# Performance work log

Measured on AMD Instinct MI355X. Metric: run time of the kernel, lower is better.

## Reference

```python
import jax, jax.numpy as jnp
import numpy as np

NUM_EXPERTS = 32
TOP_K = 4
HIDDEN = 2048
INTER = 768
N_TOKENS = 2048
NORM_TOPK = True


def setup_inputs() -> dict:
    key = jax.random.key(0)
    k0, k1, k2, k3 = jax.random.split(key, 4)
    hidden_states = jax.random.normal(k0, (N_TOKENS, HIDDEN), dtype=jnp.float32)
    # router gate: Linear(hidden, num_experts), stored as (h, E)
    Wg = jax.random.normal(k1, (HIDDEN, NUM_EXPERTS), dtype=jnp.float32) * 0.02
    # per-expert merged gate_up: (E, h, 2*i); down: (E, i, h)
    Wgu = jax.random.normal(k2, (NUM_EXPERTS, HIDDEN, 2 * INTER), dtype=jnp.float32) * 0.02
    Wd = jax.random.normal(k3, (NUM_EXPERTS, INTER, HIDDEN), dtype=jnp.float32) * 0.02
    return {"hidden_states": hidden_states, "Wg": Wg, "Wgu": Wgu, "Wd": Wd}


def reference(hidden_states, Wg, Wgu, Wd):
    E = Wgu.shape[0]
    # ---- routing ----
    router_logits = hidden_states @ Wg                       # (N, E)
    probs = jax.nn.softmax(router_logits.astype(jnp.float32), axis=-1)
    topk_w, topk_idx = jax.lax.top_k(probs, TOP_K)           # (N, K)
    if NORM_TOPK:
        topk_w = topk_w / jnp.sum(topk_w, axis=-1, keepdims=True)
    topk_w = topk_w.astype(hidden_states.dtype)
    # dense combine weights: (N, E), zero where expert not selected
    combine = jnp.einsum("nke,nk->ne", jax.nn.one_hot(topk_idx, E, dtype=topk_w.dtype), topk_w)
    # ---- experts (dense dispatch, zero-weighted combine == gather/scatter math) ----
    gate_up = jnp.einsum("nh,ehf->nef", hidden_states, Wgu)  # (N, E, 2i)
    gate, up = jnp.split(gate_up, 2, axis=-1)                # (N, E, i) each
    y = jax.nn.silu(gate) * up                               # SiluAndMul
    y = y * combine[:, :, None]                              # apply routing weight before down-proj (linear -> equivalent)
    out = jnp.einsum("nef,efh->nh", y, Wd)                   # (N, h)
    return out
```

## Files before the change

kernel.cpp:

```cpp
#include <hip/hip_runtime.h>
#include <hip/hip_bf16.h>

#define NE 32
#define TOPK 4
#define HID 2048
#define INTER 768
#define NT 2048
#define MAXTILE 96

typedef float f32x4 __attribute__((ext_vector_type(4)));
typedef float f32x2 __attribute__((ext_vector_type(2)));
typedef unsigned int u32x4 __attribute__((ext_vector_type(4)));
typedef unsigned int u32x2 __attribute__((ext_vector_type(2)));
typedef short short8 __attribute__((ext_vector_type(8)));
typedef __bf16 bf16x8 __attribute__((ext_vector_type(8)));

__device__ inline unsigned short f2bf(float f) {
  unsigned u = __builtin_bit_cast(unsigned, f);
  u += 0x7fffu + ((u >> 16) & 1u);
  return (unsigned short)(u >> 16);
}
__device__ inline unsigned pack2(unsigned short a, unsigned short b) {
  return (unsigned)a | ((unsigned)b << 16);
}
__device__ inline f32x4 mfma_bf16(short8 a, short8 b, f32x4 c) {
  return __builtin_amdgcn_mfma_f32_16x16x32_bf16(
      __builtin_bit_cast(bf16x8, a), __builtin_bit_cast(bf16x8, b), c, 0, 0, 0);
}
__device__ inline void gload16(const void* g, void* l) {
  __builtin_amdgcn_global_load_lds(
      (const __attribute__((address_space(1))) void*)g,
      (__attribute__((address_space(3))) void*)l, 16, 0, 0);
}
__device__ inline bool locate(const int* __restrict__ counts, int tile, int& e,
                              int& m0, int& base, int& ne) {
  int tl = tile;
  base = 0;
  for (e = 0; e < NE; ++e) {
    const int c = counts[e];
    const int nt = (c + 127) >> 7;
    if (tl < nt) {
      m0 = tl << 7;
      ne = c;
      return true;
    }
    tl -= nt;
    base += c;
  }
  return false;
}

__global__ __launch_bounds__(64) void k_router(const float* __restrict__ X,
                                               const float* __restrict__ Wg,
                                               int* __restrict__ expert_of,
                                               float* __restrict__ weight_of,
                                               int* __restrict__ counts,
                                               unsigned short* __restrict__ Xb) {
  const int n = blockIdx.x;
  const int lane = threadIdx.x;
  const float* x = X + (size_t)n * HID;
  float acc[NE];
#pragma unroll
  for (int e = 0; e < NE; ++e) acc[e] = 0.f;
  for (int h = lane; h < HID; h += 64) {
    const float xv = x[h];
    const f32x4* wr = (const f32x4*)(Wg + (size_t)h * NE);
#pragma unroll
    for (int q = 0; q < NE / 4; ++q) {
      f32x4 w4 = wr[q];
      acc[q * 4 + 0] += xv * w4[0];
      acc[q * 4 + 1] += xv * w4[1];
      acc[q * 4 + 2] += xv * w4[2];
      acc[q * 4 + 3] += xv * w4[3];
    }
  }
  const f32x4* x4 = (const f32x4*)x;
  u32x2* xb2 = (u32x2*)(Xb + (size_t)n * HID);
#pragma unroll
  for (int it = 0; it < HID / 4 / 64; ++it) {
    const int q = it * 64 + lane;
    f32x4 v = x4[q];
    u32x2 t = {pack2(f2bf(v[0]), f2bf(v[1])), pack2(f2bf(v[2]), f2bf(v[3]))};
    xb2[q] = t;
  }
#pragma unroll
  for (int off = 32; off >= 1; off >>= 1) {
#pragma unroll
    for (int e = 0; e < NE; ++e) acc[e] += __shfl_xor(acc[e], off, 64);
  }
  if (lane == 0) {
    float m = acc[0];
#pragma unroll
    for (int e = 1; e < NE; ++e) m = fmaxf(m, acc[e]);
    unsigned used = 0;
    int idx[TOPK];
    float wv[TOPK];
    float wsum = 0.f;
    for (int k = 0; k < TOPK; ++k) {
      int best = 0;
      float bv = -1e30f;
      for (int e = 0; e < NE; ++e) {
        if (!((used >> e) & 1u) && acc[e] > bv) { bv = acc[e]; best = e; }
      }
      used |= 1u << best;
      float w = expf(bv - m);
      idx[k] = best;
      wv[k] = w;
      wsum += w;
    }
    const float inv = 1.f / wsum;
    for (int k = 0; k < TOPK; ++k) {
      expert_of[n * TOPK + k] = idx[k];
      weight_of[n * TOPK + k] = wv[k] * inv;
      atomicAdd(&counts[idx[k]], 1);
    }
  }
}

__global__ __launch_bounds__(64) void k_scatter(const int* __restrict__ expert_of,
                                                const float* __restrict__ weight_of,
                                                const int* __restrict__ counts,
                                                int* __restrict__ slot_token,
                                                float* __restrict__ slot_w) {
  const int e = blockIdx.x;
  const int lane = threadIdx.x;
  int cnt = 0;
  for (int i = 0; i < NE; ++i) cnt += (i < e) ? counts[i] : 0;
  for (int a0 = 0; a0 < NT * TOPK; a0 += 64) {
    const int a = a0 + lane;
    const bool m = (expert_of[a] == e);
    const unsigned long long bal = __ballot(m);
    if (m) {
      const int pos = cnt + __popcll(bal & ((1ull << lane) - 1ull));
      slot_token[pos] = a >> 2;
      slot_w[pos] = weight_of[a];
    }
    cnt += __popcll(bal);
  }
}

__global__ __launch_bounds__(512, 4) void k_gemm1(
    const unsigned short* __restrict__ Xb, const float* __restrict__ Wgu,
    const int* __restrict__ slot_token, const float* __restrict__ slot_w,
    const int* __restrict__ counts, unsigned short* __restrict__ Y) {
  int e, m0, base, ne;
  if (!locate(counts, blockIdx.x, e, m0, base, ne)) return;
  const int n0 = blockIdx.y * 64;
  const int tid = threadIdx.x;
  const int lane = tid & 63, w = tid >> 6;
  const int wm = w >> 1, wn = w & 1;
  const int fr = lane & 15, fo = lane >> 4;
  const int lr = lane >> 3, lk = lane & 7;

  __shared__ __attribute__((aligned(16))) unsigned short As[2][128 * 64];
  __shared__ __attribute__((aligned(16))) unsigned short Bg[2][64 * 64];
  __shared__ __attribute__((aligned(16))) unsigned short Bu[2][64 * 64];

  f32x4 accg[2][2], accu[2][2];
#pragma unroll
  for (int i = 0; i < 2; ++i)
#pragma unroll
    for (int j = 0; j < 2; ++j) {
      f32x4 z = {0.f, 0.f, 0.f, 0.f};
      accg[i][j] = z;
      accu[i][j] = z;
    }

  const unsigned short* asrc[2];
#pragma unroll
  for (int i = 0; i < 2; ++i) {
    const int ra = (w * 2 + i) * 8 + lr;
    const int tok = slot_token[base + min(m0 + ra, ne - 1)];
    asrc[i] = Xb + (size_t)tok * HID + ((lk ^ (ra & 7)) << 3);
  }

  const int np = tid & 31, kg = (tid >> 5) & 7, rg = tid >> 8;
  const float* bsrc = Wgu + (size_t)e * HID * (2 * INTER) +
                      (size_t)(kg * 8) * (2 * INTER) + rg * INTER + n0 + 2 * np;
  const int n_a = 2 * np, n_b = 2 * np + 1;
  const int wofa = n_a * 64 + ((kg ^ (n_a & 7)) << 3);
  const int wofb = n_b * 64 + ((kg ^ (n_b & 7)) << 3);

  auto stage_a = [&](int t, int b) {
#pragma unroll
    for (int i = 0; i < 2; ++i) gload16(asrc[i] + t * 64, &As[b][(w * 2 + i) * 512]);
  };
  auto load_b = [&](int t, f32x2* bv) {
    const float* bp = bsrc + (size_t)(t * 64) * (2 * INTER);
#pragma unroll
    for (int j = 0; j < 8; ++j) bv[j] = *(const f32x2*)(bp + (size_t)j * (2 * INTER));
  };
  auto pack_write = [&](const f32x2* bv, int b) {
    u32x4 ta = {pack2(f2bf(bv[0][0]), f2bf(bv[1][0])), pack2(f2bf(bv[2][0]), f2bf(bv[3][0])),
                pack2(f2bf(bv[4][0]), f2bf(bv[5][0])), pack2(f2bf(bv[6][0]), f2bf(bv[7][0]))};
    u32x4 tb = {pack2(f2bf(bv[0][1]), f2bf(bv[1][1])), pack2(f2bf(bv[2][1]), f2bf(bv[3][1])),
                pack2(f2bf(bv[4][1]), f2bf(bv[5][1])), pack2(f2bf(bv[6][1]), f2bf(bv[7][1]))};
    unsigned short* Bd = rg ? Bu[b] : Bg[b];
    *(u32x4*)&Bd[wofa] = ta;
    *(u32x4*)&Bd[wofb] = tb;
  };
  auto do_mfma = [&](int b) {
#pragma unroll
    for (int ks = 0; ks < 2; ++ks) {
      const int c = ks * 4 + fo;
      short8 a[2], bg[2], bu[2];
#pragma unroll
      for (int mi = 0; mi < 2; ++mi) {
        const int row = wm * 32 + mi * 16 + fr;
        a[mi] = *(const short8*)&As[b][row * 64 + ((c ^ (row & 7)) << 3)];
      }
#pragma unroll
      for (int ni = 0; ni < 2; ++ni) {
        const int row = wn * 32 + ni * 16 + fr;
        const int off = row * 64 + ((c ^ (row & 7)) << 3);
        bg[ni] = *(const short8*)&Bg[b][off];
        bu[ni] = *(const short8*)&Bu[b][off];
      }
#pragma unroll
      for (int mi = 0; mi < 2; ++mi)
#pragma unroll
        for (int ni = 0; ni < 2; ++ni) {
          accg[mi][ni] = mfma_bf16(a[mi], bg[ni], accg[mi][ni]);
          accu[mi][ni] = mfma_bf16(a[mi], bu[ni], accu[mi][ni]);
        }
    }
  };

  const int NS = HID / 64;
  f32x2 bv[2][8];
  stage_a(0, 0);
  load_b(0, bv[0]);
  load_b(1, bv[1]);
  pack_write(bv[0], 0);
  asm volatile("s_waitcnt lgkmcnt(0)" ::: "memory");
  __builtin_amdgcn_s_barrier();

#pragma unroll 2
  for (int t = 0; t < NS - 2; ++t) {
    const int cur = t & 1, nxt = cur ^ 1;
    stage_a(t + 1, nxt);
    load_b(t + 2, bv[cur]);
    asm volatile("s_waitcnt vmcnt(18)" ::: "memory");
    do_mfma(cur);
    pack_write(bv[nxt], nxt);
    asm volatile("s_waitcnt lgkmcnt(0)" ::: "memory");
    __builtin_amdgcn_s_barrier();
  }
  {
    const int t = NS - 2, cur = t & 1, nxt = cur ^ 1;
    stage_a(t + 1, nxt);
    asm volatile("s_waitcnt vmcnt(10)" ::: "memory");
    do_mfma(cur);
    pack_write(bv[nxt], nxt);
    __syncthreads();
  }
  do_mfma((NS - 1) & 1);

#pragma unroll
  for (int mi = 0; mi < 2; ++mi) {
#pragma unroll
    for (int j = 0; j < 4; ++j) {
      const int gm = m0 + wm * 32 + mi * 16 + fo * 4 + j;
      if (gm < ne) {
        const float wgt = slot_w[base + gm];
        unsigned short* yp = Y + (size_t)(base + gm) * INTER + n0 + wn * 32;
#pragma unroll
        for (int ni = 0; ni < 2; ++ni) {
          const float g = accg[mi][ni][j];
          const float u = accu[mi][ni][j];
          const float yv = (g / (1.0f + __expf(-g))) * u * wgt;
          yp[ni * 16 + fr] = f2bf(yv);
        }
      }
    }
  }
}

__global__ __launch_bounds__(512, 4) void k_gemm2(
    const unsigned short* __restrict__ Y, const float* __restrict__ Wd,
    const int* __restrict__ slot_token, const int* __restrict__ counts,
    float* __restrict__ out) {
  int e, m0, base, ne;
  if (!locate(counts, blockIdx.x, e, m0, base, ne)) return;
  const int n0 = blockIdx.y * 128;
  const int tid = threadIdx.x;
  const int lane = tid & 63, w = tid >> 6;
  const int wm = w >> 1, wn = w & 1;
  const int fr = lane & 15, fo = lane >> 4;
  const int lr = lane >> 3, lk = lane & 7;

  __shared__ __attribute__((aligned(16))) unsigned short As[2][128 * 64];
  __shared__ __attribute__((aligned(16))) unsigned short Bs[2][128 * 64];

  f32x4 acc[2][4];
#pragma unroll
  for (int i = 0; i < 2; ++i)
#pragma unroll
    for (int j = 0; j < 4; ++j) {
      f32x4 z = {0.f, 0.f, 0.f, 0.f};
      acc[i][j] = z;
    }

  const unsigned short* asrc[2];
#pragma unroll
  for (int i = 0; i < 2; ++i) {
    const int ra = (w * 2 + i) * 8 + lr;
    const int grow = base + min(m0 + ra, ne - 1);
    asrc[i] = Y + (size_t)grow * INTER + ((lk ^ (ra & 7)) << 3);
  }

  const int np = tid & 63, kg = tid >> 6;
  const float* bsrc = Wd + (size_t)e * INTER * HID + (size_t)(kg * 8) * HID + n0 + 2 * np;
  const int n_a = 2 * np, n_b = 2 * np + 1;
  const int wofa = n_a * 64 + ((kg ^ (n_a & 7)) << 3);
  const int wofb = n_b * 64 + ((kg ^ (n_b & 7)) << 3);

  auto stage_a = [&](int t, int b) {
#pragma unroll
    for (int i = 0; i < 2; ++i) gload16(asrc[i] + t * 64, &As[b][(w * 2 + i) * 512]);
  };
  auto load_b = [&](int t, f32x2* bv) {
    const float* bp = bsrc + (size_t)(t * 64) * HID;
#pragma unroll
    for (int j = 0; j < 8; ++j) bv[j] = *(const f32x2*)(bp + (size_t)j * HID);
  };
  auto pack_write = [&](const f32x2* bv, int b) {
    u32x4 ta = {pack2(f2bf(bv[0][0]), f2bf(bv[1][0])), pack2(f2bf(bv[2][0]), f2bf(bv[3][0])),
                pack2(f2bf(bv[4][0]), f2bf(bv[5][0])), pack2(f2bf(bv[6][0]), f2bf(bv[7][0]))};
    u32x4 tb = {pack2(f2bf(bv[0][1]), f2bf(bv[1][1])), pack2(f2bf(bv[2][1]), f2bf(bv[3][1])),
                pack2(f2bf(bv[4][1]), f2bf(bv[5][1])), pack2(f2bf(bv[6][1]), f2bf(bv[7][1]))};
    *(u32x4*)&Bs[b][wofa] = ta;
    *(u32x4*)&Bs[b][wofb] = tb;
  };
  auto do_mfma = [&](int b) {
#pragma unroll
    for (int ks = 0; ks < 2; ++ks) {
      const int c = ks * 4 + fo;
      short8 a[2], bb[4];
#pragma unroll
      for (int mi = 0; mi < 2; ++mi) {
        const int row = wm * 32 + mi * 16 + fr;
        a[mi] = *(const short8*)&As[b][row * 64 + ((c ^ (row & 7)) << 3)];
      }
#pragma unroll
      for (int ni = 0; ni < 4; ++ni) {
        const int row = wn * 64 + ni * 16 + fr;
        bb[ni] = *(const short8*)&Bs[b][row * 64 + ((c ^ (row & 7)) << 3)];
      }
#pragma unroll
      for (int mi = 0; mi < 2; ++mi)
#pragma unroll
        for (int ni = 0; ni < 4; ++ni) acc[mi][ni] = mfma_bf16(a[mi], bb[ni], acc[mi][ni]);
    }
  };

  const int NS = INTER / 64;
  f32x2 bv[2][8];
  stage_a(0, 0);
  load_b(0, bv[0]);
  load_b(1, bv[1]);
  pack_write(bv[0], 0);
  asm volatile("s_waitcnt lgkmcnt(0)" ::: "memory");
  __builtin_amdgcn_s_barrier();

#pragma unroll 2
  for (int t = 0; t < NS - 2; ++t) {
    const int cur = t & 1, nxt = cur ^ 1;
    stage_a(t + 1, nxt);
    load_b(t + 2, bv[cur]);
    asm volatile("s_waitcnt vmcnt(18)" ::: "memory");
    do_mfma(cur);
    pack_write(bv[nxt], nxt);
    asm volatile("s_waitcnt lgkmcnt(0)" ::: "memory");
    __builtin_amdgcn_s_barrier();
  }
  {
    const int t = NS - 2, cur = t & 1, nxt = cur ^ 1;
    stage_a(t + 1, nxt);
    asm volatile("s_waitcnt vmcnt(10)" ::: "memory");
    do_mfma(cur);
    pack_write(bv[nxt], nxt);
    __syncthreads();
  }
  do_mfma((NS - 1) & 1);

#pragma unroll
  for (int mi = 0; mi < 2; ++mi) {
#pragma unroll
    for (int j = 0; j < 4; ++j) {
      const int gm = m0 + wm * 32 + mi * 16 + fo * 4 + j;
      if (gm < ne) {
        const int tok = slot_token[base + gm];
        float* op = out + (size_t)tok * HID + n0 + wn * 64;
#pragma unroll
        for (int ni = 0; ni < 4; ++ni) atomicAdd(&op[ni * 16 + fr], acc[mi][ni][j]);
      }
    }
  }
}

extern "C" void kernel_launch(void* const* d_in, const int* in_sizes, int n_in,
                              void* d_out, int out_size, void* d_ws, size_t ws_size,
                              hipStream_t stream) {
  (void)in_sizes; (void)n_in; (void)ws_size;
  const float* X = (const float*)d_in[0];
  const float* Wg = (const float*)d_in[1];
  const float* Wgu = (const float*)d_in[2];
  const float* Wd = (const float*)d_in[3];
  float* out = (float*)d_out;

  char* ws = (char*)d_ws;
  int* counts = (int*)(ws + 0);
  int* expert_of = (int*)(ws + 2048);
  float* weight_of = (float*)(ws + 2048 + 32768);
  int* slot_token = (int*)(ws + 2048 + 2 * 32768);
  float* slot_w = (float*)(ws + 2048 + 3 * 32768);
  unsigned short* Xb = (unsigned short*)(ws + 133120);
  unsigned short* Yb = (unsigned short*)(ws + 8521728);

  hipMemsetAsync(counts, 0, 128, stream);
  hipMemsetAsync(d_out, 0, (size_t)out_size * sizeof(float), stream);

  k_router<<<NT, 64, 0, stream>>>(X, Wg, expert_of, weight_of, counts, Xb);
  k_scatter<<<NE, 64, 0, stream>>>(expert_of, weight_of, counts, slot_token, slot_w);
  k_gemm1<<<dim3(MAXTILE, INTER / 64), 512, 0, stream>>>(Xb, Wgu, slot_token, slot_w,
                                                         counts, Yb);
  k_gemm2<<<dim3(MAXTILE, HID / 128), 512, 0, stream>>>(Yb, Wd, slot_token, counts, out);
}
```

Baseline: 508.2 us.

## Use 256-row expert tiles with K=32 stages and fuse output zeroing into router

Both expert GEMMs move from 128-row tiles to 256-row tiles (MAXTILE 96→64), so each fp32 weight tile fetched and converted to bf16 is reused by twice as many tokens. The K step shrinks from 64 to 32 to keep LDS within budget, and the B tile uses a padded stride of 40 instead of an XOR swizzle. MFMA sections are wrapped in s_setprio. The output memset is folded into the router kernel. In exchange there are twice as many pipeline iterations and barriers, more accumulator registers per thread, and more wasted padding rows for experts with few tokens.

```diff
diff --git a/kernel.cpp b/kernel.cpp
--- a/kernel.cpp
+++ b/kernel.cpp
@@ -6,7 +6,7 @@
 #define HID 2048
 #define INTER 768
 #define NT 2048
-#define MAXTILE 96
+#define MAXTILE 64
 
 typedef float f32x4 __attribute__((ext_vector_type(4)));
 typedef float f32x2 __attribute__((ext_vector_type(2)));
@@ -38,9 +38,9 @@
   base = 0;
   for (e = 0; e < NE; ++e) {
     const int c = counts[e];
-    const int nt = (c + 127) >> 7;
+    const int nt = (c + 255) >> 8;
     if (tl < nt) {
-      m0 = tl << 7;
+      m0 = tl << 8;
       ne = c;
       return true;
     }
@@ -55,10 +55,16 @@
                                                int* __restrict__ expert_of,
                                                float* __restrict__ weight_of,
                                                int* __restrict__ counts,
-                                               unsigned short* __restrict__ Xb) {
+                                               unsigned short* __restrict__ Xb,
+                                               float* __restrict__ out) {
   const int n = blockIdx.x;
   const int lane = threadIdx.x;
   const float* x = X + (size_t)n * HID;
+  f32x4* orow = (f32x4*)(out + (size_t)n * HID);
+  const f32x4 z4 = {0.f, 0.f, 0.f, 0.f};
+#pragma unroll
+  for (int i = 0; i < HID / 4 / 64; ++i) orow[i * 64 + lane] = z4;
+
   float acc[NE];
 #pragma unroll
   for (int e = 0; e < NE; ++e) acc[e] = 0.f;
@@ -150,15 +156,14 @@
   const int lane = tid & 63, w = tid >> 6;
   const int wm = w >> 1, wn = w & 1;
   const int fr = lane & 15, fo = lane >> 4;
-  const int lr = lane >> 3, lk = lane & 7;
-
-  __shared__ __attribute__((aligned(16))) unsigned short As[2][128 * 64];
-  __shared__ __attribute__((aligned(16))) unsigned short Bg[2][64 * 64];
-  __shared__ __attribute__((aligned(16))) unsigned short Bu[2][64 * 64];
-
-  f32x4 accg[2][2], accu[2][2];
-#pragma unroll
-  for (int i = 0; i < 2; ++i)
+
+  __shared__ __attribute__((aligned(16))) unsigned short As[2][256 * 32];
+  __shared__ __attribute__((aligned(16))) unsigned short Bg[2][64 * 40];
+  __shared__ __attribute__((aligned(16))) unsigned short Bu[2][64 * 40];
+
+  f32x4 accg[4][2], accu[4][2];
+#pragma unroll
+  for (int i = 0; i < 4; ++i)
 #pragma unroll
     for (int j = 0; j < 2; ++j) {
       f32x4 z = {0.f, 0.f, 0.f, 0.f};
@@ -169,65 +174,62 @@
   const unsigned short* asrc[2];
 #pragma unroll
   for (int i = 0; i < 2; ++i) {
-    const int ra = (w * 2 + i) * 8 + lr;
+    const int ra = (w * 2 + i) * 16 + (lane >> 2);
     const int tok = slot_token[base + min(m0 + ra, ne - 1)];
-    asrc[i] = Xb + (size_t)tok * HID + ((lk ^ (ra & 7)) << 3);
+    asrc[i] = Xb + (size_t)tok * HID + (((lane & 3) ^ (ra & 3)) << 3);
   }
 
   const int np = tid & 31, kg = (tid >> 5) & 7, rg = tid >> 8;
   const float* bsrc = Wgu + (size_t)e * HID * (2 * INTER) +
-                      (size_t)(kg * 8) * (2 * INTER) + rg * INTER + n0 + 2 * np;
-  const int n_a = 2 * np, n_b = 2 * np + 1;
-  const int wofa = n_a * 64 + ((kg ^ (n_a & 7)) << 3);
-  const int wofb = n_b * 64 + ((kg ^ (n_b & 7)) << 3);
+                      (size_t)(kg * 4) * (2 * INTER) + rg * INTER + n0 + 2 * np;
+  const int wofa = (2 * np) * 40 + kg * 4;
+  const int wofb = (2 * np + 1) * 40 + kg * 4;
 
   auto stage_a = [&](int t, int b) {
 #pragma unroll
-    for (int i = 0; i < 2; ++i) gload16(asrc[i] + t * 64, &As[b][(w * 2 + i) * 512]);
+    for (int i = 0; i < 2; ++i) gload16(asrc[i] + t * 32, &As[b][(w * 2 + i) * 512]);
   };
   auto load_b = [&](int t, f32x2* bv) {
-    const float* bp = bsrc + (size_t)(t * 64) * (2 * INTER);
-#pragma unroll
-    for (int j = 0; j < 8; ++j) bv[j] = *(const f32x2*)(bp + (size_t)j * (2 * INTER));
+    const float* bp = bsrc + (size_t)(t * 32) * (2 * INTER);
+#pragma unroll
+    for (int j = 0; j < 4; ++j) bv[j] = *(const f32x2*)(bp + (size_t)j * (2 * INTER));
   };
   auto pack_write = [&](const f32x2* bv, int b) {
-    u32x4 ta = {pack2(f2bf(bv[0][0]), f2bf(bv[1][0])), pack2(f2bf(bv[2][0]), f2bf(bv[3][0])),
-                pack2(f2bf(bv[4][0]), f2bf(bv[5][0])), pack2(f2bf(bv[6][0]), f2bf(bv[7][0]))};
-    u32x4 tb = {pack2(f2bf(bv[0][1]), f2bf(bv[1][1])), pack2(f2bf(bv[2][1]), f2bf(bv[3][1])),
-                pack2(f2bf(bv[4][1]), f2bf(bv[5][1])), pack2(f2bf(bv[6][1]), f2bf(bv[7][1]))};
+    u32x2 lo = {pack2(f2bf(bv[0][0]), f2bf(bv[1][0])),
+                pack2(f2bf(bv[2][0]), f2bf(bv[3][0]))};
+    u32x2 hi = {pack2(f2bf(bv[0][1]), f2bf(bv[1][1])),
+                pack2(f2bf(bv[2][1]), f2bf(bv[3][1]))};
     unsigned short* Bd = rg ? Bu[b] : Bg[b];
-    *(u32x4*)&Bd[wofa] = ta;
-    *(u32x4*)&Bd[wofb] = tb;
+    *(u32x2*)&Bd[wofa] = lo;
+    *(u32x2*)&Bd[wofb] = hi;
   };
   auto do_mfma = [&](int b) {
-#pragma unroll
-    for (int ks = 0; ks < 2; ++ks) {
-      const int c = ks * 4 + fo;
-      short8 a[2], bg[2], bu[2];
-#pragma unroll
-      for (int mi = 0; mi < 2; ++mi) {
-        const int row = wm * 32 + mi * 16 + fr;
-        a[mi] = *(const short8*)&As[b][row * 64 + ((c ^ (row & 7)) << 3)];
+    short8 a[4], bgf[2], buf[2];
+#pragma unroll
+    for (int mi = 0; mi < 4; ++mi) {
+      const int row = wm * 64 + mi * 16 + fr;
+      a[mi] = *(const short8*)&As[b][row * 32 + ((fo ^ (row & 3)) << 3)];
+    }
+#pragma unroll
+    for (int ni = 0; ni < 2; ++ni) {
+      const int row = wn * 32 + ni * 16 + fr;
+      const int off = row * 40 + (fo << 3);
+      bgf[ni] = *(const short8*)&Bg[b][off];
+      buf[ni] = *(const short8*)&Bu[b][off];
+    }
+    __builtin_amdgcn_s_setprio(1);
+#pragma unroll
+    for (int mi = 0; mi < 4; ++mi)
+#pragma unroll
+      for (int ni = 0; ni < 2; ++ni) {
+        accg[mi][ni] = mfma_bf16(a[mi], bgf[ni], accg[mi][ni]);
+        accu[mi][ni] = mfma_bf16(a[mi], buf[ni], accu[mi][ni]);
       }
-#pragma unroll
-      for (int ni = 0; ni < 2; ++ni) {
-        const int row = wn * 32 + ni * 16 + fr;
-        const int off = row * 64 + ((c ^ (row & 7)) << 3);
-        bg[ni] = *(const short8*)&Bg[b][off];
-        bu[ni] = *(const short8*)&Bu[b][off];
-      }
-#pragma unroll
-      for (int mi = 0; mi < 2; ++mi)
-#pragma unroll
-        for (int ni = 0; ni < 2; ++ni) {
-          accg[mi][ni] = mfma_bf16(a[mi], bg[ni], accg[mi][ni]);
-          accu[mi][ni] = mfma_bf16(a[mi], bu[ni], accu[mi][ni]);
-        }
-    }
-  };
-
-  const int NS = HID / 64;
-  f32x2 bv[2][8];
+    __builtin_amdgcn_s_setprio(0);
+  };
+
+  const int NS = HID / 32;
+  f32x2 bv[2][4];
   stage_a(0, 0);
   load_b(0, bv[0]);
   load_b(1, bv[1]);
@@ -240,27 +242,29 @@
     const int cur = t & 1, nxt = cur ^ 1;
     stage_a(t + 1, nxt);
     load_b(t + 2, bv[cur]);
-    asm volatile("s_waitcnt vmcnt(18)" ::: "memory");
+    asm volatile("s_waitcnt vmcnt(10)" ::: "memory");
     do_mfma(cur);
     pack_write(bv[nxt], nxt);
     asm volatile("s_waitcnt lgkmcnt(0)" ::: "memory");
     __builtin_amdgcn_s_barrier();
   }
   {
-    const int t = NS - 2, cur = t & 1, nxt = cur ^ 1;
-    stage_a(t + 1, nxt);
-    asm volatile("s_waitcnt vmcnt(10)" ::: "memory");
+    const int cur = (NS - 2) & 1, nxt = cur ^ 1;
+    stage_a(NS - 1, nxt);
+    asm volatile("s_waitcnt vmcnt(6)" ::: "memory");
     do_mfma(cur);
     pack_write(bv[nxt], nxt);
-    __syncthreads();
-  }
+    asm volatile("s_waitcnt lgkmcnt(0)" ::: "memory");
+    __builtin_amdgcn_s_barrier();
+  }
+  asm volatile("s_waitcnt vmcnt(0)" ::: "memory");
   do_mfma((NS - 1) & 1);
 
 #pragma unroll
-  for (int mi = 0; mi < 2; ++mi) {
+  for (int mi = 0; mi < 4; ++mi) {
 #pragma unroll
     for (int j = 0; j < 4; ++j) {
-      const int gm = m0 + wm * 32 + mi * 16 + fo * 4 + j;
+      const int gm = m0 + wm * 64 + mi * 16 + fo * 4 + j;
       if (gm < ne) {
         const float wgt = slot_w[base + gm];
         unsigned short* yp = Y + (size_t)(base + gm) * INTER + n0 + wn * 32;
@@ -287,14 +291,13 @@
   const int lane = tid & 63, w = tid >> 6;
   const int wm = w >> 1, wn = w & 1;
   const int fr = lane & 15, fo = lane >> 4;
-  const int lr = lane >> 3, lk = lane & 7;
-
-  __shared__ __attribute__((aligned(16))) unsigned short As[2][128 * 64];
-  __shared__ __attribute__((aligned(16))) unsigned short Bs[2][128 * 64];
-
-  f32x4 acc[2][4];
-#pragma unroll
-  for (int i = 0; i < 2; ++i)
+
+  __shared__ __attribute__((aligned(16))) unsigned short As[2][256 * 32];
+  __shared__ __attribute__((aligned(16))) unsigned short Bs[2][128 * 40];
+
+  f32x4 acc[4][4];
+#pragma unroll
+  for (int i = 0; i < 4; ++i)
 #pragma unroll
     for (int j = 0; j < 4; ++j) {
       f32x4 z = {0.f, 0.f, 0.f, 0.f};
@@ -304,58 +307,55 @@
   const unsigned short* asrc[2];
 #pragma unroll
   for (int i = 0; i < 2; ++i) {
-    const int ra = (w * 2 + i) * 8 + lr;
+    const int ra = (w * 2 + i) * 16 + (lane >> 2);
     const int grow = base + min(m0 + ra, ne - 1);
-    asrc[i] = Y + (size_t)grow * INTER + ((lk ^ (ra & 7)) << 3);
-  }
-
-  const int np = tid & 63, kg = tid >> 6;
-  const float* bsrc = Wd + (size_t)e * INTER * HID + (size_t)(kg * 8) * HID + n0 + 2 * np;
-  const int n_a = 2 * np, n_b = 2 * np + 1;
-  const int wofa = n_a * 64 + ((kg ^ (n_a & 7)) << 3);
-  const int wofb = n_b * 64 + ((kg ^ (n_b & 7)) << 3);
+    asrc[i] = Y + (size_t)grow * INTER + (((lane & 3) ^ (ra & 3)) << 3);
+  }
+
+  const int np = tid & 63, kg = (tid >> 6) & 7;
+  const float* bsrc = Wd + (size_t)e * INTER * HID + (size_t)(kg * 4) * HID + n0 + 2 * np;
+  const int wofa = (2 * np) * 40 + kg * 4;
+  const int wofb = (2 * np + 1) * 40 + kg * 4;
 
   auto stage_a = [&](int t, int b) {
 #pragma unroll
-    for (int i = 0; i < 2; ++i) gload16(asrc[i] + t * 64, &As[b][(w * 2 + i) * 512]);
+    for (int i = 0; i < 2; ++i) gload16(asrc[i] + t * 32, &As[b][(w * 2 + i) * 512]);
   };
   auto load_b = [&](int t, f32x2* bv) {
-    const float* bp = bsrc + (size_t)(t * 64) * HID;
-#pragma unroll
-    for (int j = 0; j < 8; ++j) bv[j] = *(const f32x2*)(bp + (size_t)j * HID);
+    const float* bp = bsrc + (size_t)(t * 32) * HID;
+#pragma unroll
+    for (int j = 0; j < 4; ++j) bv[j] = *(const f32x2*)(bp + (size_t)j * HID);
   };
   auto pack_write = [&](const f32x2* bv, int b) {
-    u32x4 ta = {pack2(f2bf(bv[0][0]), f2bf(bv[1][0])), pack2(f2bf(bv[2][0]), f2bf(bv[3][0])),
-                pack2(f2bf(bv[4][0]), f2bf(bv[5][0])), pack2(f2bf(bv[6][0]), f2bf(bv[7][0]))};
-    u32x4 tb = {pack2(f2bf(bv[0][1]), f2bf(bv[1][1])), pack2(f2bf(bv[2][1]), f2bf(bv[3][1])),
-                pack2(f2bf(bv[4][1]), f2bf(bv[5][1])), pack2(f2bf(bv[6][1]), f2bf(bv[7][1]))};
-    *(u32x4*)&Bs[b][wofa] = ta;
-    *(u32x4*)&Bs[b][wofb] = tb;
+    u32x2 lo = {pack2(f2bf(bv[0][0]), f2bf(bv[1][0])),
+                pack2(f2bf(bv[2][0]), f2bf(bv[3][0]))};
+    u32x2 hi = {pack2(f2bf(bv[0][1]), f2bf(bv[1][1])),
+                pack2(f2bf(bv[2][1]), f2bf(bv[3][1]))};
+    *(u32x2*)&Bs[b][wofa] = lo;
+    *(u32x2*)&Bs[b][wofb] = hi;
   };
   auto do_mfma = [&](int b) {
-#pragma unroll
-    for (int ks = 0; ks < 2; ++ks) {
-      const int c = ks * 4 + fo;
-      short8 a[2], bb[4];
-#pragma unroll
-      for (int mi = 0; mi < 2; ++mi) {
-        const int row = wm * 32 + mi * 16 + fr;
-        a[mi] = *(const short8*)&As[b][row * 64 + ((c ^ (row & 7)) << 3)];
-      }
-#pragma unroll
-      for (int ni = 0; ni < 4; ++ni) {
-        const int row = wn * 64 + ni * 16 + fr;
-        bb[ni] = *(const short8*)&Bs[b][row * 64 + ((c ^ (row & 7)) << 3)];
-      }
-#pragma unroll
-      for (int mi = 0; mi < 2; ++mi)
-#pragma unroll
-        for (int ni = 0; ni < 4; ++ni) acc[mi][ni] = mfma_bf16(a[mi], bb[ni], acc[mi][ni]);
-    }
-  };
-
-  const int NS = INTER / 64;
-  f32x2 bv[2][8];
+    short8 a[4], bb[4];
+#pragma unroll
+    for (int mi = 0; mi < 4; ++mi) {
+      const int row = wm * 64 + mi * 16 + fr;
+      a[mi] = *(const short8*)&As[b][row * 32 + ((fo ^ (row & 3)) << 3)];
+    }
+#pragma unroll
+    for (int ni = 0; ni < 4; ++ni) {
+      const int row = wn * 64 + ni * 16 + fr;
+      bb[ni] = *(const short8*)&Bs[b][row * 40 + (fo << 3)];
+    }
+    __builtin_amdgcn_s_setprio(1);
+#pragma unroll
+    for (int mi = 0; mi < 4; ++mi)
+#pragma unroll
+      for (int ni = 0; ni < 4; ++ni) acc[mi][ni] = mfma_bf16(a[mi], bb[ni], acc[mi][ni]);
+    __builtin_amdgcn_s_setprio(0);
+  };
+
+  const int NS = INTER / 32;
+  f32x2 bv[2][4];
   stage_a(0, 0);
   load_b(0, bv[0]);
   load_b(1, bv[1]);
@@ -368,27 +368,29 @@
     const int cur = t & 1, nxt = cur ^ 1;
     stage_a(t + 1, nxt);
     load_b(t + 2, bv[cur]);
-    asm volatile("s_waitcnt vmcnt(18)" ::: "memory");
+    asm volatile("s_waitcnt vmcnt(10)" ::: "memory");
     do_mfma(cur);
     pack_write(bv[nxt], nxt);
     asm volatile("s_waitcnt lgkmcnt(0)" ::: "memory");
     __builtin_amdgcn_s_barrier();
   }
   {
-    const int t = NS - 2, cur = t & 1, nxt = cur ^ 1;
-    stage_a(t + 1, nxt);
-    asm volatile("s_waitcnt vmcnt(10)" ::: "memory");
+    const int cur = (NS - 2) & 1, nxt = cur ^ 1;
+    stage_a(NS - 1, nxt);
+    asm volatile("s_waitcnt vmcnt(6)" ::: "memory");
     do_mfma(cur);
     pack_write(bv[nxt], nxt);
-    __syncthreads();
-  }
+    asm volatile("s_waitcnt lgkmcnt(0)" ::: "memory");
+    __builtin_amdgcn_s_barrier();
+  }
+  asm volatile("s_waitcnt vmcnt(0)" ::: "memory");
   do_mfma((NS - 1) & 1);
 
 #pragma unroll
-  for (int mi = 0; mi < 2; ++mi) {
+  for (int mi = 0; mi < 4; ++mi) {
 #pragma unroll
     for (int j = 0; j < 4; ++j) {
-      const int gm = m0 + wm * 32 + mi * 16 + fo * 4 + j;
+      const int gm = m0 + wm * 64 + mi * 16 + fo * 4 + j;
       if (gm < ne) {
         const int tok = slot_token[base + gm];
         float* op = out + (size_t)tok * HID + n0 + wn * 64;
@@ -402,7 +404,7 @@
 extern "C" void kernel_launch(void* const* d_in, const int* in_sizes, int n_in,
                               void* d_out, int out_size, void* d_ws, size_t ws_size,
                               hipStream_t stream) {
-  (void)in_sizes; (void)n_in; (void)ws_size;
+  (void)in_sizes; (void)n_in; (void)ws_size; (void)out_size;
   const float* X = (const float*)d_in[0];
   const float* Wg = (const float*)d_in[1];
   const float* Wgu = (const float*)d_in[2];
@@ -419,9 +421,8 @@
   unsigned short* Yb = (unsigned short*)(ws + 8521728);
 
   hipMemsetAsync(counts, 0, 128, stream);
-  hipMemsetAsync(d_out, 0, (size_t)out_size * sizeof(float), stream);
-
-  k_router<<<NT, 64, 0, stream>>>(X, Wg, expert_of, weight_of, counts, Xb);
+
+  k_router<<<NT, 64, 0, stream>>>(X, Wg, expert_of, weight_of, counts, Xb, out);
   k_scatter<<<NE, 64, 0, stream>>>(expert_of, weight_of, counts, slot_token, slot_w);
   k_gemm1<<<dim3(MAXTILE, INTER / 64), 512, 0, stream>>>(Xb, Wgu, slot_token, slot_w,
                                                          counts, Yb);
```

Result: slower. 572.3 us (+12.6%).
